# Kernel optimization log

Measured on AMD Instinct MI355X. Metric: run time of the kernel, lower is better.

The kernel has to match this reference:

```python
import jax, jax.numpy as jnp
import numpy as np

# Module config (matches init_kwargs)
P_THRESH = 0.9
IOU_THRESH = 0.5
WIDTH, HEIGHT = 3072, 2304
NUM_PATCHES = 96
XPS = WIDTH // NUM_PATCHES   # 32, math.floor(width / num_of_patches)
YPS = HEIGHT // NUM_PATCHES  # 24


def setup_inputs() -> dict:
    key = jax.random.key(0)
    x = jax.random.uniform(key, (5, NUM_PATCHES, NUM_PATCHES), dtype=jnp.float32)
    return {"x": x}


def reference(x):
    """Fixed-shape JAX version of ReduceBoundingBoxes.forward.

    Returns out: [N, 5] rows (score, x, y, w, h) sorted by descending score;
    rows not surviving (prob threshold + greedy NMS) are zeroed.
    (Torch returns only the kept rows; here kept rows appear first, in the
    same order, with identical values, followed by zero rows.)
    """
    P, Q = x.shape[1], x.shape[2]
    N = P * Q
    dt = x.dtype
    ii = (jnp.arange(P, dtype=dt) * XPS)[:, None]  # i * x_patch_size
    jj = (jnp.arange(Q, dtype=dt) * YPS)[None, :]  # j * y_patch_size

    prob = x[0]
    # convert_batch_bbx_to_xyxy_scaled (applied everywhere; only rows passing
    # the prob threshold survive, identical to torch's masked in-place update)
    bx1 = x[1] * WIDTH + ii
    by1 = x[2] * HEIGHT + jj
    bx2 = (x[3] - x[1]) * WIDTH + ii
    by2 = (x[4] - x[2]) * HEIGHT + jj

    boxes = jnp.stack([bx1, by1, bx2, by2], axis=-1).reshape(N, 4)
    scores = prob.reshape(N)
    valid = scores > P_THRESH

    # Sort by descending score; invalid boxes sink to the end.
    order = jnp.argsort(-jnp.where(valid, scores, -jnp.inf))
    boxes_s = boxes[order]
    scores_s = scores[order]
    valid_s = valid[order]

    x1, y1, x2, y2 = boxes_s[:, 0], boxes_s[:, 1], boxes_s[:, 2], boxes_s[:, 3]
    area = (x2 - x1) * (y2 - y1)
    # Pairwise IoU (torchvision convention, no +1). [N, N] -- dominant buffer.
    iw = jnp.clip(jnp.minimum(x2[:, None], x2[None, :]) - jnp.maximum(x1[:, None], x1[None, :]), 0.0)
    ih = jnp.clip(jnp.minimum(y2[:, None], y2[None, :]) - jnp.maximum(y1[:, None], y1[None, :]), 0.0)
    inter = iw * ih
    iou = inter / (area[:, None] + area[None, :] - inter + 1e-9)

    # Greedy NMS: sequential suppression in score order.
    idx = jnp.arange(N)

    def body(i, keep):
        sup = keep[i] & (iou[i] > IOU_THRESH) & (idx > i)
        return keep & ~sup

    keep = jax.lax.fori_loop(0, N, body, valid_s)

    # convert_batch_to_xywh on (score, x1, y1, x2, y2)
    out = jnp.stack([scores_s, x1, y1, x2 - x1, y2 - y1], axis=-1)
    out = jnp.where(keep[:, None], out, jnp.zeros((), dtype=dt))
    return out
```

## Files before the change

kernel.cpp:

```cpp
#pragma clang fp contract(off)
#include <hip/hip_runtime.h>

#define NP 96
#define N_TOT (NP * NP)
#define FWIDTH 3072.0f
#define FHEIGHT 2304.0f
#define XPS 32
#define YPS 24
#define VMAX 1024
typedef unsigned long long u64;

#define WS_CNT   0
#define WS_SX1   64
#define WS_SY1   4160
#define WS_SX2   8256
#define WS_SY2   12352
#define WS_SAR   16448
#define WS_SSC   20544
#define WS_MSK   24640

__global__ __launch_bounds__(256)
void k_sort(const float* __restrict__ x, unsigned int* __restrict__ cnt,
            float* __restrict__ sx1, float* __restrict__ sy1,
            float* __restrict__ sx2, float* __restrict__ sy2,
            float* __restrict__ sar, float* __restrict__ ssc) {
    __shared__ u64 lk[VMAX];
    __shared__ unsigned int wcnt[4];
    __shared__ int part[256];
    const int t = threadIdx.x;
    const int lane = t & 63;
    const int w = t >> 6;
    const int rbase = w * 2304;

    unsigned int cw = 0;
    for (int i = 0; i < 36; ++i) {
        float s = x[rbase + (i << 6) + lane];
        cw += (unsigned int)__popcll(__ballot(s > 0.9f));
    }
    if (lane == 0) wcnt[w] = cw;
    __syncthreads();
    unsigned int off = 0;
    for (int ww = 0; ww < w; ++ww) off += wcnt[ww];
    const unsigned int V4 = wcnt[0] + wcnt[1] + wcnt[2] + wcnt[3];
    const int V = (V4 > VMAX) ? VMAX : (int)V4;
    if (blockIdx.x == 0 && t == 0) *cnt = (unsigned int)V;

    const u64 below = (lane == 0) ? 0ull : (~0ull >> (64 - lane));
    unsigned int base = off;
    for (int i = 0; i < 36; ++i) {
        const int n = rbase + (i << 6) + lane;
        const float s = x[n];
        const bool v = s > 0.9f;
        const u64 m = __ballot(v ? 1 : 0);
        if (v) {
            unsigned int pos = base + (unsigned int)__popcll(m & below);
            if (pos < VMAX) {
                unsigned int bits = __float_as_uint(s);
                lk[pos] = ((u64)(~bits) << 32) | (unsigned int)n;
            }
        }
        base += (unsigned int)__popcll(m);
    }
    for (int i = V + t; i < VMAX; i += 256) lk[i] = ~0ULL;
    __syncthreads();

    const int p = (blockIdx.x << 6) + (t & 63);
    const int seg = t >> 6;
    const u64 mykey = lk[p];
    int c = 0;
    const int sbase = seg << 8;
    #pragma unroll 8
    for (int k = 0; k < 256; ++k)
        c += (lk[sbase + k] < mykey) ? 1 : 0;
    part[t] = c;
    __syncthreads();

    if (t < 64 && p < V) {
        int rank = part[t] + part[t + 64] + part[t + 128] + part[t + 192];
        u64 key = mykey;
        unsigned int n = (unsigned int)(key & 0xffffffffu);
        float score = __uint_as_float(~(unsigned int)(key >> 32));
        int pi = (int)n / NP, pj = (int)n % NP;
        float fi = (float)(pi * XPS);
        float fj = (float)(pj * YPS);
        float v1 = x[1 * N_TOT + n];
        float v2 = x[2 * N_TOT + n];
        float v3 = x[3 * N_TOT + n];
        float v4 = x[4 * N_TOT + n];
        float bx1 = __fadd_rn(__fmul_rn(v1, FWIDTH), fi);
        float by1 = __fadd_rn(__fmul_rn(v2, FHEIGHT), fj);
        float bx2 = __fadd_rn(__fmul_rn(__fsub_rn(v3, v1), FWIDTH), fi);
        float by2 = __fadd_rn(__fmul_rn(__fsub_rn(v4, v2), FHEIGHT), fj);
        sx1[rank] = bx1; sy1[rank] = by1; sx2[rank] = bx2; sy2[rank] = by2;
        sar[rank]  = __fmul_rn(__fsub_rn(bx2, bx1), __fsub_rn(by2, by1));
        ssc[rank]  = score;
    }
}

__global__ __launch_bounds__(64)
void k_masks(const float* __restrict__ sx1, const float* __restrict__ sy1,
             const float* __restrict__ sx2, const float* __restrict__ sy2,
             const float* __restrict__ sar, u64* __restrict__ msk,
             float* __restrict__ out) {
    const int b = blockIdx.x;
    const int cj = b >> 4;
    const int w  = b & 15;
    const int lane = threadIdx.x;
    if (w > cj) {
        int r = cj * 15 - (cj * (cj - 1)) / 2 + (w - cj - 1);
        int t = (r << 6) + lane;
        for (int i = VMAX * 5 + t; i < N_TOT * 5; i += 7680)
            out[i] = 0.0f;
        return;
    }
    __shared__ float qx1[64], qy1[64], qx2[64], qy2[64], qa[64];
    const int ibase = w << 6;
    qx1[lane] = sx1[ibase + lane];
    qy1[lane] = sy1[ibase + lane];
    qx2[lane] = sx2[ibase + lane];
    qy2[lane] = sy2[ibase + lane];
    qa[lane]  = sar[ibase + lane];
    const int j = (cj << 6) + lane;
    const float bx1 = sx1[j], by1 = sy1[j], bx2 = sx2[j], by2 = sy2[j], barea = sar[j];
    __syncthreads();

    u64 bits = 0ull;
    #pragma unroll 4
    for (int m = 0; m < 64; ++m) {
        const int im = ibase + m;
        float iw = fmaxf(__fsub_rn(fminf(qx2[m], bx2), fmaxf(qx1[m], bx1)), 0.0f);
        float ih = fmaxf(__fsub_rn(fminf(qy2[m], by2), fmaxf(qy1[m], by1)), 0.0f);
        float inter = __fmul_rn(iw, ih);
        float denom = __fadd_rn(__fsub_rn(__fadd_rn(qa[m], barea), inter), 1e-9f);
        bool pred = (im < j) && ((inter / denom) > 0.5f);
        bits |= ((u64)(pred ? 1u : 0u)) << m;
    }
    msk[(w << 10) + j] = bits;
}

__global__ __launch_bounds__(1024)
void k_resolve(const float* __restrict__ sx1, const float* __restrict__ sy1,
               const float* __restrict__ sx2, const float* __restrict__ sy2,
               const float* __restrict__ ssc, const unsigned int* __restrict__ cntp,
               const u64* __restrict__ msk, float* __restrict__ out) {
    __shared__ u64 savail[16], sD[16];
    const int tid = threadIdx.x;
    const int lane = tid & 63;
    const int wid = tid >> 6;
    const int V = (int)*cntp;
    const bool valid = (tid < V);

    const float x1 = sx1[tid], y1 = sy1[tid], x2 = sx2[tid], y2 = sy2[tid], sc = ssc[tid];

    u64 colw[16];
    #pragma unroll
    for (int c = 0; c < 16; ++c)
        colw[c] = (c <= wid) ? msk[(c << 10) + tid] : 0ull;

    u64 w0 = __ballot(valid ? 1 : 0);
    if (lane == 0) savail[wid] = w0;
    __syncthreads();

    bool kept = false;
    for (;;) {
        u64 av[16]; u64 any = 0ull;
        #pragma unroll
        for (int c = 0; c < 16; ++c) { av[c] = savail[c]; any |= av[c]; }
        if (any == 0ull) break;
        const bool in_avail = valid && ((av[wid] >> lane) & 1ull);
        u64 conf = 0ull;
        for (int c = 0; c <= wid; ++c) conf |= (colw[c] & av[c]);
        const bool isD = in_avail && (conf == 0ull);
        u64 Dw = __ballot(isD ? 1 : 0);
        if (lane == 0) sD[wid] = Dw;
        __syncthreads();
        u64 confD = 0ull;
        for (int c = 0; c <= wid; ++c) confD |= (colw[c] & sD[c]);
        if (isD) kept = true;
        const bool drop = in_avail && (isD || confD != 0ull);
        u64 dropw = __ballot(drop ? 1 : 0);
        if (lane == 0) savail[wid] = av[wid] & ~dropw;
        __syncthreads();
    }

    float o0 = 0.f, o1 = 0.f, o2 = 0.f, o3 = 0.f, o4 = 0.f;
    if (kept) {
        o0 = sc;
        o1 = x1;
        o2 = y1;
        o3 = __fsub_rn(x2, x1);
        o4 = __fsub_rn(y2, y1);
    }
    out[tid * 5 + 0] = o0;
    out[tid * 5 + 1] = o1;
    out[tid * 5 + 2] = o2;
    out[tid * 5 + 3] = o3;
    out[tid * 5 + 4] = o4;
}

extern "C" void kernel_launch(void* const* d_in, const int* in_sizes, int n_in,
                              void* d_out, int out_size, void* d_ws, size_t ws_size,
                              hipStream_t stream) {
    const float* x = (const float*)d_in[0];
    float* out = (float*)d_out;
    char* ws = (char*)d_ws;
    unsigned int* cnt = (unsigned int*)(ws + WS_CNT);
    float* sx1 = (float*)(ws + WS_SX1);
    float* sy1 = (float*)(ws + WS_SY1);
    float* sx2 = (float*)(ws + WS_SX2);
    float* sy2 = (float*)(ws + WS_SY2);
    float* sar = (float*)(ws + WS_SAR);
    float* ssc = (float*)(ws + WS_SSC);
    u64*   msk = (u64*)(ws + WS_MSK);

    hipLaunchKernelGGL(k_sort,    dim3(VMAX / 64), dim3(256),  0, stream,
                       x, cnt, sx1, sy1, sx2, sy2, sar, ssc);
    hipLaunchKernelGGL(k_masks,   dim3(256),       dim3(64),   0, stream,
                       sx1, sy1, sx2, sy2, sar, msk, out);
    hipLaunchKernelGGL(k_resolve, dim3(1),         dim3(1024), 0, stream,
                       sx1, sy1, sx2, sy2, ssc, cnt, msk, out);
}
```

Measured before the change: 80.62 us.

## Fuse sort, mask and resolve kernels into one cooperative kernel with grid syncs

Replaces the three separate launches (sort, IoU mask build, greedy resolve) with a single cooperative kernel of 16 blocks of 1024 threads, using grid.sync between phases. This is meant to remove launch and inter-kernel gap overhead, and it also widens each sort block to 16 waves so the rank count splits into 16 segments. In exchange it relies on cooperative-launch grid barriers, which carry their own cost, and the mask phase now runs on only 16 blocks instead of 256.

```diff
diff --git a/kernel.cpp b/kernel.cpp
--- a/kernel.cpp
+++ b/kernel.cpp
@@ -1,5 +1,7 @@
 #pragma clang fp contract(off)
 #include <hip/hip_runtime.h>
+#include <hip/hip_cooperative_groups.h>
+namespace cg = cooperative_groups;
 
 #define NP 96
 #define N_TOT (NP * NP)
@@ -10,44 +12,50 @@
 #define VMAX 1024
 typedef unsigned long long u64;
 
-#define WS_CNT   0
-#define WS_SX1   64
-#define WS_SY1   4160
-#define WS_SX2   8256
-#define WS_SY2   12352
-#define WS_SAR   16448
-#define WS_SSC   20544
-#define WS_MSK   24640
-
-__global__ __launch_bounds__(256)
-void k_sort(const float* __restrict__ x, unsigned int* __restrict__ cnt,
-            float* __restrict__ sx1, float* __restrict__ sy1,
-            float* __restrict__ sx2, float* __restrict__ sy2,
-            float* __restrict__ sar, float* __restrict__ ssc) {
+#define WS_SX1   0
+#define WS_SY1   4096
+#define WS_SX2   8192
+#define WS_SY2   12288
+#define WS_SAR   16384
+#define WS_SSC   20480
+#define WS_MSK   24576
+
+__global__ __launch_bounds__(1024)
+void k_all(const float* __restrict__ x, float* __restrict__ out,
+           u64* __restrict__ msk,
+           float* __restrict__ sx1, float* __restrict__ sy1,
+           float* __restrict__ sx2, float* __restrict__ sy2,
+           float* __restrict__ sar, float* __restrict__ ssc) {
+    cg::grid_group grid = cg::this_grid();
     __shared__ u64 lk[VMAX];
-    __shared__ unsigned int wcnt[4];
-    __shared__ int part[256];
+    __shared__ int part[1024];
+    __shared__ unsigned int wcnt[16];
+    __shared__ int sV;
+    __shared__ float qx1[16][64], qy1[16][64], qx2[16][64], qy2[16][64], qa[16][64];
+    __shared__ u64 savail[16], sD[16];
+
     const int t = threadIdx.x;
     const int lane = t & 63;
-    const int w = t >> 6;
-    const int rbase = w * 2304;
-
+    const int wid = t >> 6;
+    const int bid = blockIdx.x;
+
+    const int rbase = wid * 576;
     unsigned int cw = 0;
-    for (int i = 0; i < 36; ++i) {
+    for (int i = 0; i < 9; ++i) {
         float s = x[rbase + (i << 6) + lane];
         cw += (unsigned int)__popcll(__ballot(s > 0.9f));
     }
-    if (lane == 0) wcnt[w] = cw;
+    if (lane == 0) wcnt[wid] = cw;
     __syncthreads();
-    unsigned int off = 0;
-    for (int ww = 0; ww < w; ++ww) off += wcnt[ww];
-    const unsigned int V4 = wcnt[0] + wcnt[1] + wcnt[2] + wcnt[3];
-    const int V = (V4 > VMAX) ? VMAX : (int)V4;
-    if (blockIdx.x == 0 && t == 0) *cnt = (unsigned int)V;
+    unsigned int off = 0, tot = 0;
+    #pragma unroll
+    for (int ww = 0; ww < 16; ++ww) { if (ww < wid) off += wcnt[ww]; tot += wcnt[ww]; }
+    const int V = (tot > VMAX) ? VMAX : (int)tot;
+    if (t == 0) sV = V;
 
     const u64 below = (lane == 0) ? 0ull : (~0ull >> (64 - lane));
     unsigned int base = off;
-    for (int i = 0; i < 36; ++i) {
+    for (int i = 0; i < 9; ++i) {
         const int n = rbase + (i << 6) + lane;
         const float s = x[n];
         const bool v = s > 0.9f;
@@ -61,22 +69,23 @@
         }
         base += (unsigned int)__popcll(m);
     }
-    for (int i = V + t; i < VMAX; i += 256) lk[i] = ~0ULL;
+    for (int i = V + t; i < VMAX; i += 1024) lk[i] = ~0ULL;
     __syncthreads();
 
-    const int p = (blockIdx.x << 6) + (t & 63);
-    const int seg = t >> 6;
+    const int p = (bid << 6) + lane;
     const u64 mykey = lk[p];
-    int c = 0;
-    const int sbase = seg << 8;
+    int cnt_lt = 0;
+    const int sbase = wid << 6;
     #pragma unroll 8
-    for (int k = 0; k < 256; ++k)
-        c += (lk[sbase + k] < mykey) ? 1 : 0;
-    part[t] = c;
+    for (int k = 0; k < 64; ++k)
+        cnt_lt += (lk[sbase + k] < mykey) ? 1 : 0;
+    part[t] = cnt_lt;
     __syncthreads();
 
     if (t < 64 && p < V) {
-        int rank = part[t] + part[t + 64] + part[t + 128] + part[t + 192];
+        int rank = 0;
+        #pragma unroll
+        for (int sg = 0; sg < 16; ++sg) rank += part[t + (sg << 6)];
         u64 key = mykey;
         unsigned int n = (unsigned int)(key & 0xffffffffu);
         float score = __uint_as_float(~(unsigned int)(key >> 32));
@@ -95,107 +104,88 @@
         sar[rank]  = __fmul_rn(__fsub_rn(bx2, bx1), __fsub_rn(by2, by1));
         ssc[rank]  = score;
     }
-}
-
-__global__ __launch_bounds__(64)
-void k_masks(const float* __restrict__ sx1, const float* __restrict__ sy1,
-             const float* __restrict__ sx2, const float* __restrict__ sy2,
-             const float* __restrict__ sar, u64* __restrict__ msk,
-             float* __restrict__ out) {
-    const int b = blockIdx.x;
-    const int cj = b >> 4;
-    const int w  = b & 15;
-    const int lane = threadIdx.x;
-    if (w > cj) {
-        int r = cj * 15 - (cj * (cj - 1)) / 2 + (w - cj - 1);
-        int t = (r << 6) + lane;
-        for (int i = VMAX * 5 + t; i < N_TOT * 5; i += 7680)
-            out[i] = 0.0f;
-        return;
-    }
-    __shared__ float qx1[64], qy1[64], qx2[64], qy2[64], qa[64];
-    const int ibase = w << 6;
-    qx1[lane] = sx1[ibase + lane];
-    qy1[lane] = sy1[ibase + lane];
-    qx2[lane] = sx2[ibase + lane];
-    qy2[lane] = sy2[ibase + lane];
-    qa[lane]  = sar[ibase + lane];
-    const int j = (cj << 6) + lane;
-    const float bx1 = sx1[j], by1 = sy1[j], bx2 = sx2[j], by2 = sy2[j], barea = sar[j];
-    __syncthreads();
-
-    u64 bits = 0ull;
-    #pragma unroll 4
-    for (int m = 0; m < 64; ++m) {
-        const int im = ibase + m;
-        float iw = fmaxf(__fsub_rn(fminf(qx2[m], bx2), fmaxf(qx1[m], bx1)), 0.0f);
-        float ih = fmaxf(__fsub_rn(fminf(qy2[m], by2), fmaxf(qy1[m], by1)), 0.0f);
-        float inter = __fmul_rn(iw, ih);
-        float denom = __fadd_rn(__fsub_rn(__fadd_rn(qa[m], barea), inter), 1e-9f);
-        bool pred = (im < j) && ((inter / denom) > 0.5f);
-        bits |= ((u64)(pred ? 1u : 0u)) << m;
-    }
-    msk[(w << 10) + j] = bits;
-}
-
-__global__ __launch_bounds__(1024)
-void k_resolve(const float* __restrict__ sx1, const float* __restrict__ sy1,
-               const float* __restrict__ sx2, const float* __restrict__ sy2,
-               const float* __restrict__ ssc, const unsigned int* __restrict__ cntp,
-               const u64* __restrict__ msk, float* __restrict__ out) {
-    __shared__ u64 savail[16], sD[16];
-    const int tid = threadIdx.x;
-    const int lane = tid & 63;
-    const int wid = tid >> 6;
-    const int V = (int)*cntp;
-    const bool valid = (tid < V);
-
-    const float x1 = sx1[tid], y1 = sy1[tid], x2 = sx2[tid], y2 = sy2[tid], sc = ssc[tid];
-
-    u64 colw[16];
-    #pragma unroll
-    for (int c = 0; c < 16; ++c)
-        colw[c] = (c <= wid) ? msk[(c << 10) + tid] : 0ull;
-
-    u64 w0 = __ballot(valid ? 1 : 0);
-    if (lane == 0) savail[wid] = w0;
-    __syncthreads();
-
-    bool kept = false;
-    for (;;) {
-        u64 av[16]; u64 any = 0ull;
+
+    const int gtid = (bid << 10) + t;
+    for (int i = VMAX * 5 + gtid; i < N_TOT * 5; i += 16384) out[i] = 0.0f;
+
+    __threadfence();
+    grid.sync();
+
+    if (wid <= bid) {
+        const int ibase = wid << 6;
+        qx1[wid][lane] = sx1[ibase + lane];
+        qy1[wid][lane] = sy1[ibase + lane];
+        qx2[wid][lane] = sx2[ibase + lane];
+        qy2[wid][lane] = sy2[ibase + lane];
+        qa [wid][lane] = sar[ibase + lane];
+        const int j = (bid << 6) + lane;
+        const float bx1 = sx1[j], by1 = sy1[j], bx2 = sx2[j], by2 = sy2[j], barea = sar[j];
+        u64 bits = 0ull;
+        #pragma unroll 4
+        for (int m = 0; m < 64; ++m) {
+            const int im = ibase + m;
+            float iw = fmaxf(__fsub_rn(fminf(qx2[wid][m], bx2), fmaxf(qx1[wid][m], bx1)), 0.0f);
+            float ih = fmaxf(__fsub_rn(fminf(qy2[wid][m], by2), fmaxf(qy1[wid][m], by1)), 0.0f);
+            float inter = __fmul_rn(iw, ih);
+            float denom = __fadd_rn(__fsub_rn(__fadd_rn(qa[wid][m], barea), inter), 1e-9f);
+            bool pred = (im < j) && ((inter / denom) > 0.5f);
+            bits |= ((u64)(pred ? 1u : 0u)) << m;
+        }
+        msk[(wid << 10) + j] = bits;
+    }
+
+    __threadfence();
+    grid.sync();
+
+    if (bid == 0) {
+        const int V3 = sV;
+        const bool valid = (t < V3);
+        const float x1 = sx1[t], y1 = sy1[t], x2 = sx2[t], y2 = sy2[t], sc = ssc[t];
+        u64 colw[16];
         #pragma unroll
-        for (int c = 0; c < 16; ++c) { av[c] = savail[c]; any |= av[c]; }
-        if (any == 0ull) break;
-        const bool in_avail = valid && ((av[wid] >> lane) & 1ull);
-        u64 conf = 0ull;
-        for (int c = 0; c <= wid; ++c) conf |= (colw[c] & av[c]);
-        const bool isD = in_avail && (conf == 0ull);
-        u64 Dw = __ballot(isD ? 1 : 0);
-        if (lane == 0) sD[wid] = Dw;
+        for (int c = 0; c < 16; ++c)
+            colw[c] = (c <= wid) ? msk[(c << 10) + t] : 0ull;
+
+        u64 w0 = __ballot(valid ? 1 : 0);
+        if (lane == 0) savail[wid] = w0;
         __syncthreads();
-        u64 confD = 0ull;
-        for (int c = 0; c <= wid; ++c) confD |= (colw[c] & sD[c]);
-        if (isD) kept = true;
-        const bool drop = in_avail && (isD || confD != 0ull);
-        u64 dropw = __ballot(drop ? 1 : 0);
-        if (lane == 0) savail[wid] = av[wid] & ~dropw;
-        __syncthreads();
-    }
-
-    float o0 = 0.f, o1 = 0.f, o2 = 0.f, o3 = 0.f, o4 = 0.f;
-    if (kept) {
-        o0 = sc;
-        o1 = x1;
-        o2 = y1;
-        o3 = __fsub_rn(x2, x1);
-        o4 = __fsub_rn(y2, y1);
-    }
-    out[tid * 5 + 0] = o0;
-    out[tid * 5 + 1] = o1;
-    out[tid * 5 + 2] = o2;
-    out[tid * 5 + 3] = o3;
-    out[tid * 5 + 4] = o4;
+
+        bool kept = false;
+        for (;;) {
+            u64 av[16]; u64 any = 0ull;
+            #pragma unroll
+            for (int c = 0; c < 16; ++c) { av[c] = savail[c]; any |= av[c]; }
+            if (any == 0ull) break;
+            const bool in_avail = valid && ((av[wid] >> lane) & 1ull);
+            u64 conf = 0ull;
+            for (int c = 0; c <= wid; ++c) conf |= (colw[c] & av[c]);
+            const bool isD = in_avail && (conf == 0ull);
+            u64 Dw = __ballot(isD ? 1 : 0);
+            if (lane == 0) sD[wid] = Dw;
+            __syncthreads();
+            u64 confD = 0ull;
+            for (int c = 0; c <= wid; ++c) confD |= (colw[c] & sD[c]);
+            if (isD) kept = true;
+            const bool drop = in_avail && (isD || confD != 0ull);
+            u64 dropw = __ballot(drop ? 1 : 0);
+            if (lane == 0) savail[wid] = av[wid] & ~dropw;
+            __syncthreads();
+        }
+
+        float o0 = 0.f, o1 = 0.f, o2 = 0.f, o3 = 0.f, o4 = 0.f;
+        if (kept) {
+            o0 = sc;
+            o1 = x1;
+            o2 = y1;
+            o3 = __fsub_rn(x2, x1);
+            o4 = __fsub_rn(y2, y1);
+        }
+        out[t * 5 + 0] = o0;
+        out[t * 5 + 1] = o1;
+        out[t * 5 + 2] = o2;
+        out[t * 5 + 3] = o3;
+        out[t * 5 + 4] = o4;
+    }
 }
 
 extern "C" void kernel_launch(void* const* d_in, const int* in_sizes, int n_in,
@@ -204,7 +194,6 @@
     const float* x = (const float*)d_in[0];
     float* out = (float*)d_out;
     char* ws = (char*)d_ws;
-    unsigned int* cnt = (unsigned int*)(ws + WS_CNT);
     float* sx1 = (float*)(ws + WS_SX1);
     float* sy1 = (float*)(ws + WS_SY1);
     float* sx2 = (float*)(ws + WS_SX2);
@@ -213,10 +202,8 @@
     float* ssc = (float*)(ws + WS_SSC);
     u64*   msk = (u64*)(ws + WS_MSK);
 
-    hipLaunchKernelGGL(k_sort,    dim3(VMAX / 64), dim3(256),  0, stream,
-                       x, cnt, sx1, sy1, sx2, sy2, sar, ssc);
-    hipLaunchKernelGGL(k_masks,   dim3(256),       dim3(64),   0, stream,
-                       sx1, sy1, sx2, sy2, sar, msk, out);
-    hipLaunchKernelGGL(k_resolve, dim3(1),         dim3(1024), 0, stream,
-                       sx1, sy1, sx2, sy2, ssc, cnt, msk, out);
+    void* args[] = { (void*)&x, (void*)&out, (void*)&msk,
+                     (void*)&sx1, (void*)&sy1, (void*)&sx2, (void*)&sy2,
+                     (void*)&sar, (void*)&ssc };
+    hipLaunchCooperativeKernel((const void*)k_all, dim3(16), dim3(1024), args, 0, stream);
 }
```

Measured after the change: 109.0 us. 1.35x slower.
